# Kernel optimization log

Hardware: AMD Instinct MI355X
Metric: run time of the kernel (lower is better)

The kernel has to match this reference:

```python
import jax, jax.numpy as jnp
import numpy as np

B, T = 2, 2048
V, C, H = 32000, 1024, 16
HS = C // H  # 64
W_SCALE = 0.02


def setup_inputs() -> dict:
    key = jax.random.key(0)
    ks = jax.random.split(key, 8)
    x = jax.random.randint(ks[0], (B, T), 0, V)
    tok_emb = jax.random.normal(ks[1], (V, C), jnp.float32) * W_SCALE
    pos_emb = jax.random.normal(ks[2], (T, C), jnp.float32) * W_SCALE
    wq = jax.random.normal(ks[3], (H, C, HS), jnp.float32) * W_SCALE
    wk = jax.random.normal(ks[4], (H, C, HS), jnp.float32) * W_SCALE
    wv = jax.random.normal(ks[5], (H, C, HS), jnp.float32) * W_SCALE
    bq = jnp.zeros((H, HS), jnp.float32)
    bk = jnp.zeros((H, HS), jnp.float32)
    bv = jnp.zeros((H, HS), jnp.float32)
    w_head = jax.random.normal(ks[6], (C, V), jnp.float32) * W_SCALE
    b_head = jnp.zeros((V,), jnp.float32)
    return dict(x=x, tok_emb=tok_emb, pos_emb=pos_emb, wq=wq, bq=bq,
                wk=wk, bk=bk, wv=wv, bv=bv, w_head=w_head, b_head=b_head)


def reference(x, tok_emb, pos_emb, wq, bq, wk, bk, wv, bv, w_head, b_head):
    Bx, Tx = x.shape
    Cx = tok_emb.shape[1]
    h = tok_emb[x] + pos_emb[:Tx]  # [B,T,C]
    # all heads batched: per-head Linear layers stacked on leading H axis
    q = jnp.einsum('btc,hcd->bhtd', h, wq) + bq[None, :, None, :]
    k = jnp.einsum('btc,hcd->bhtd', h, wk) + bk[None, :, None, :]
    v = jnp.einsum('btc,hcd->bhtd', h, wv) + bv[None, :, None, :]
    # NOTE: original scales by n_embd**-0.5 (full C), not head_size**-0.5
    att = jnp.einsum('bhtd,bhsd->bhts', q, k) * (Cx ** -0.5)
    causal = jnp.tril(jnp.ones((Tx, Tx), dtype=bool))
    att = jnp.where(causal, att, jnp.finfo(att.dtype).min)
    att = jax.nn.softmax(att, axis=-1)
    y = jnp.einsum('bhts,bhsd->bhtd', att, v)  # [B,H,T,HS]
    y = jnp.transpose(y, (0, 2, 1, 3)).reshape(Bx, Tx, Cx)  # concat heads
    logits = jnp.einsum('btc,cv->btv', y, w_head) + b_head  # [B,T,V]
    return logits
```

## Files before the change

### kernel.cpp

```cpp
#include <hip/hip_runtime.h>

#define T_SEQ 2048
#define C_DIM 1024
#define H_N   16
#define HS_D  64
#define V_DIM 32000

typedef float f32x4 __attribute__((ext_vector_type(4)));
typedef __bf16 bf16x8 __attribute__((ext_vector_type(8)));
typedef unsigned short us4 __attribute__((ext_vector_type(4)));
typedef unsigned short us8 __attribute__((ext_vector_type(8)));

__device__ inline unsigned short f2bf(float f) {
  unsigned int u = __float_as_uint(f);
  u = (u + 0x7FFFu + ((u >> 16) & 1u)) >> 16;
  return (unsigned short)u;
}

__global__ __launch_bounds__(256) void embed_kernel(
    const int* __restrict__ x, const float* __restrict__ tok,
    const float* __restrict__ pos, unsigned short* __restrict__ h) {
  int idx = blockIdx.x * 256 + threadIdx.x;
  int bt = idx >> 8;
  int c4 = (idx & 255) * 4;
  int t = bt & (T_SEQ - 1);
  int tokid = x[bt];
  f32x4 a = *(const f32x4*)(tok + (size_t)tokid * C_DIM + c4);
  f32x4 b = *(const f32x4*)(pos + (size_t)t * C_DIM + c4);
  f32x4 s = a + b;
  us4 o;
  o[0] = f2bf(s[0]); o[1] = f2bf(s[1]); o[2] = f2bf(s[2]); o[3] = f2bf(s[3]);
  *(us4*)(h + (size_t)bt * C_DIM + c4) = o;
}

__global__ __launch_bounds__(256) void repack_qkv(
    const float* __restrict__ wq, const float* __restrict__ wk, const float* __restrict__ wv,
    const float* __restrict__ bq, const float* __restrict__ bk, const float* __restrict__ bv,
    unsigned short* __restrict__ wt, float* __restrict__ biasp) {
  int which = blockIdx.y;
  const float* w = (which == 0) ? wq : (which == 1) ? wk : wv;
  int i = blockIdx.x * 256 + threadIdx.x;
  int d = i & 63;
  int c = (i >> 6) & (C_DIM - 1);
  int hh = i >> 16;
  int n = which * 1024 + hh * 64 + d;
  wt[(size_t)n * C_DIM + c] = f2bf(w[i]);
  if (c == 0) {
    const float* bb = (which == 0) ? bq : (which == 1) ? bk : bv;
    biasp[n] = bb[hh * 64 + d];
  }
}

__global__ __launch_bounds__(256) void repack_whead(
    const float* __restrict__ wh, unsigned short* __restrict__ wht) {
  __shared__ float tile[64][65];
  int v0 = blockIdx.x * 64;
  int c0 = blockIdx.y * 64;
  int tr = threadIdx.x >> 6;
  int tc = threadIdx.x & 63;
#pragma unroll
  for (int i = 0; i < 16; ++i) {
    int r = i * 4 + tr;
    tile[r][tc] = wh[(size_t)(c0 + r) * V_DIM + v0 + tc];
  }
  __syncthreads();
#pragma unroll
  for (int i = 0; i < 16; ++i) {
    int vr = i * 4 + tr;
    wht[(size_t)(v0 + vr) * C_DIM + c0 + tc] = f2bf(tile[tc][vr]);
  }
}

__global__ __launch_bounds__(256) void gemm_bf16_o16(
    const unsigned short* __restrict__ A, const unsigned short* __restrict__ Bt,
    const float* __restrict__ bias, unsigned short* __restrict__ Cout, int N, int Mtiles) {
  const int K = 1024;
  __shared__ unsigned short As[128 * 32];
  __shared__ unsigned short Bs[128 * 32];
  int tid = threadIdx.x;
  int lane = tid & 63, wvi = tid >> 6;
  int cpx = gridDim.x >> 3;
  int lin = blockIdx.x;
  int wg = (lin & 7) * cpx + (lin >> 3);
  int m0 = (wg % Mtiles) * 128;
  int n0 = (wg / Mtiles) * 128;
  int wmm = (wvi >> 1) * 64, wnn = (wvi & 1) * 64;
  int r16 = lane & 15, gg = lane >> 4;
  f32x4 acc[4][4] = {};

  for (int k0 = 0; k0 < K; k0 += 32) {
#pragma unroll
    for (int it = 0; it < 2; ++it) {
      int ch = it * 256 + wvi * 64 + lane;
      int row = ch >> 2, cc = (ch & 3) * 8;
      const unsigned short* ga = A + (size_t)(m0 + row) * K + k0 + cc;
      __builtin_amdgcn_global_load_lds(
          (const __attribute__((address_space(1))) void*)ga,
          (__attribute__((address_space(3))) void*)&As[ch * 8], 16, 0, 0);
      const unsigned short* gb = Bt + (size_t)(n0 + row) * K + k0 + cc;
      __builtin_amdgcn_global_load_lds(
          (const __attribute__((address_space(1))) void*)gb,
          (__attribute__((address_space(3))) void*)&Bs[ch * 8], 16, 0, 0);
    }
    __syncthreads();
    bf16x8 fa[4], fb[4];
#pragma unroll
    for (int m = 0; m < 4; ++m)
      fa[m] = *(const bf16x8*)&As[(wmm + m * 16 + r16) * 32 + gg * 8];
#pragma unroll
    for (int n = 0; n < 4; ++n)
      fb[n] = *(const bf16x8*)&Bs[(wnn + n * 16 + r16) * 32 + gg * 8];
#pragma unroll
    for (int m = 0; m < 4; ++m)
#pragma unroll
      for (int n = 0; n < 4; ++n)
        acc[m][n] = __builtin_amdgcn_mfma_f32_16x16x32_bf16(fa[m], fb[n], acc[m][n], 0, 0, 0);
    __syncthreads();
  }
#pragma unroll
  for (int m = 0; m < 4; ++m) {
    int row = m0 + wmm + m * 16 + gg * 4;
#pragma unroll
    for (int n = 0; n < 4; ++n) {
      int col = n0 + wnn + n * 16 + r16;
      float bval = bias[col];
#pragma unroll
      for (int j = 0; j < 4; ++j)
        Cout[(size_t)(row + j) * N + col] = f2bf(acc[m][n][j] + bval);
    }
  }
}

__global__ __launch_bounds__(256) void transpose_v(
    const unsigned short* __restrict__ qkv, unsigned short* __restrict__ vt) {
  __shared__ unsigned short tile[64][72];
  int bh = blockIdx.y;
  int b = bh >> 4, h = bh & 15;
  int tb = blockIdx.x;
  int r = threadIdx.x >> 2;
  int c0 = (threadIdx.x & 3) * 16;
  const unsigned short* src = qkv + ((size_t)(b * T_SEQ) + tb * 64 + r) * 3072 + 2048 + h * 64 + c0;
  *(us8*)&tile[r][c0] = *(const us8*)src;
  *(us8*)&tile[r][c0 + 8] = *(const us8*)(src + 8);
  __syncthreads();
  unsigned short* dst = vt + (size_t)bh * 64 * T_SEQ + (size_t)r * T_SEQ + tb * 64 + c0;
  us8 o1, o2;
#pragma unroll
  for (int i = 0; i < 8; ++i) { o1[i] = tile[c0 + i][r]; o2[i] = tile[c0 + 8 + i][r]; }
  *(us8*)dst = o1;
  *(us8*)(dst + 8) = o2;
}

#define GK 1024
#define GNT 16

__global__ __launch_bounds__(512, 1) void gemm256(
    const unsigned short* __restrict__ A, const unsigned short* __restrict__ Bt,
    const float* __restrict__ bias, float* __restrict__ Cout, int N, int Mtiles) {
  __shared__ unsigned short As[2][256 * 64];
  __shared__ unsigned short Bs[2][256 * 64];
  int tid = threadIdx.x;
  int lane = tid & 63;
  int wid = tid >> 6;
  int wm = wid >> 2, wn = wid & 3;
  int l16 = lane & 15, g = lane >> 4;
  int swz = l16 & 7;

  int cpx = gridDim.x >> 3;
  int lin = blockIdx.x;
  int wg = (lin & 7) * cpx + (lin >> 3);
  int m0 = (wg % Mtiles) * 256;
  int n0 = (wg / Mtiles) * 256;

  auto stageA2 = [&](int kt, int mh) {
    unsigned short* lds = As[kt & 1];
#pragma unroll
    for (int q = 0; q < 2; ++q) {
      int chunk = q * 512 + tid;
      int rr = chunk >> 3;
      int row = (rr & 63) + ((rr >> 6) << 7) + mh * 64;
      int cpos = chunk & 7;
      int c = cpos ^ (row & 7);
      const unsigned short* src = A + (size_t)(m0 + row) * GK + kt * 64 + c * 8;
      __builtin_amdgcn_global_load_lds(
          (const __attribute__((address_space(1))) void*)src,
          (__attribute__((address_space(3))) void*)(lds + row * 64 + cpos * 8), 16, 0, 0);
    }
  };
  auto stageB4 = [&](int kt) {
    unsigned short* lds = Bs[kt & 1];
#pragma unroll
    for (int q = 0; q < 4; ++q) {
      int chunk = q * 512 + tid;
      int row = chunk >> 3;
      int cpos = chunk & 7;
      int c = cpos ^ (row & 7);
      const unsigned short* src = Bt + (size_t)(n0 + row) * GK + kt * 64 + c * 8;
      __builtin_amdgcn_global_load_lds(
          (const __attribute__((address_space(1))) void*)src,
          (__attribute__((address_space(3))) void*)(lds + row * 64 + cpos * 8), 16, 0, 0);
    }
  };

  stageA2(0, 0); stageB4(0);
  stageA2(0, 1);
  stageA2(1, 0); stageB4(1);
  asm volatile("s_waitcnt vmcnt(8)" ::: "memory");
  asm volatile("s_barrier" ::: "memory");

  f32x4 acc[8][4] = {};

  for (int t = 0; t < GNT; ++t) {
    const char* Ab = (const char*)As[t & 1];
    const char* Bb = (const char*)Bs[t & 1];
    bf16x8 bA[4][2], bB[4][2];

#pragma unroll
    for (int mi = 0; mi < 4; ++mi) {
      int row = wm * 128 + mi * 16 + l16;
#pragma unroll
      for (int kk = 0; kk < 2; ++kk)
        bA[mi][kk] = *(const bf16x8*)(Ab + row * 128 + (((kk * 4 + g) ^ swz) * 16));
    }
#pragma unroll
    for (int ni = 0; ni < 4; ++ni) {
      int row = wn * 64 + ni * 16 + l16;
#pragma unroll
      for (int kk = 0; kk < 2; ++kk)
        bB[ni][kk] = *(const bf16x8*)(Bb + row * 128 + (((kk * 4 + g) ^ swz) * 16));
    }
    if (t + 1 < GNT) stageA2(t + 1, 1);
    asm volatile("s_barrier" ::: "memory");
    asm volatile("s_waitcnt lgkmcnt(0)" ::: "memory");
    __builtin_amdgcn_sched_barrier(0);
    __builtin_amdgcn_s_setprio(1);
#pragma unroll
    for (int mi = 0; mi < 4; ++mi)
#pragma unroll
      for (int ni = 0; ni < 4; ++ni)
#pragma unroll
        for (int kk = 0; kk < 2; ++kk)
          acc[mi][ni] = __builtin_amdgcn_mfma_f32_16x16x32_bf16(bB[ni][kk], bA[mi][kk], acc[mi][ni], 0, 0, 0);
    __builtin_amdgcn_s_setprio(0);
    if (t + 1 < GNT) asm volatile("s_waitcnt vmcnt(8)" ::: "memory");
    else             asm volatile("s_waitcnt vmcnt(0)" ::: "memory");
    asm volatile("s_barrier" ::: "memory");

#pragma unroll
    for (int mi = 0; mi < 4; ++mi) {
      int row = wm * 128 + 64 + mi * 16 + l16;
#pragma unroll
      for (int kk = 0; kk < 2; ++kk)
        bA[mi][kk] = *(const bf16x8*)(Ab + row * 128 + (((kk * 4 + g) ^ swz) * 16));
    }
    if (t + 2 < GNT) { stageA2(t + 2, 0); stageB4(t + 2); }
    asm volatile("s_barrier" ::: "memory");
    asm volatile("s_waitcnt lgkmcnt(0)" ::: "memory");
    __builtin_amdgcn_sched_barrier(0);
    __builtin_amdgcn_s_setprio(1);
#pragma unroll
    for (int mi = 0; mi < 4; ++mi)
#pragma unroll
      for (int ni = 0; ni < 4; ++ni)
#pragma unroll
        for (int kk = 0; kk < 2; ++kk)
          acc[4 + mi][ni] = __builtin_amdgcn_mfma_f32_16x16x32_bf16(bB[ni][kk], bA[mi][kk], acc[4 + mi][ni], 0, 0, 0);
    __builtin_amdgcn_s_setprio(0);
    if (t + 2 < GNT)       asm volatile("s_waitcnt vmcnt(8)" ::: "memory");
    else if (t + 2 == GNT) asm volatile("s_waitcnt vmcnt(2)" ::: "memory");
    asm volatile("s_barrier" ::: "memory");
  }

#pragma unroll
  for (int mf = 0; mf < 8; ++mf) {
    int row = m0 + wm * 128 + mf * 16 + l16;
    float* outp = Cout + (size_t)row * N + n0 + wn * 64;
#pragma unroll
    for (int ni = 0; ni < 4; ++ni) {
      f32x4 v = acc[mf][ni];
      f32x4 bv = *(const f32x4*)&bias[n0 + wn * 64 + ni * 16 + g * 4];
      v += bv;
      __builtin_nontemporal_store(v, (f32x4*)(outp + ni * 16 + g * 4));
    }
  }
}

__global__ __launch_bounds__(256) void attn_mfma(
    const unsigned short* __restrict__ qkv, const unsigned short* __restrict__ vt,
    unsigned short* __restrict__ y) {
  __shared__ unsigned short Kl[2][4096];
  __shared__ unsigned short Vl[2][4096];
  __shared__ char Pl[8192];

  int bh = blockIdx.y;
  int b = bh >> 4, h = bh & 15;
  int qb = (T_SEQ / 64 - 1) - blockIdx.x;
  int tid = threadIdx.x;
  int lane = tid & 63, w = tid >> 6;
  int l16 = lane & 15, g = lane >> 4;
  size_t bT = (size_t)b * T_SEQ;
  const float scale2 = 0.03125f * 1.44269504f;

  const unsigned short* qrow = qkv + (bT + qb * 64 + w * 16 + l16) * 3072 + h * 64;
  bf16x8 qf[2] = { *(const bf16x8*)(qrow + g * 8), *(const bf16x8*)(qrow + 32 + g * 8) };

  f32x4 yacc[4] = {};
  float mrun[4], lrun[4];
#pragma unroll
  for (int j = 0; j < 4; ++j) { mrun[j] = -3.0e38f; lrun[j] = 0.f; }

  auto stageK = [&](int kb, int buf) {
    const unsigned short* base = qkv + (bT + kb * 64) * 3072 + 1024 + h * 64;
#pragma unroll
    for (int q2 = 0; q2 < 2; ++q2) {
      int chunk = q2 * 256 + tid;
      int row = chunk >> 3, cpos = chunk & 7;
      int c = cpos ^ (row & 7);
      const unsigned short* src = base + (size_t)row * 3072 + c * 8;
      __builtin_amdgcn_global_load_lds(
          (const __attribute__((address_space(1))) void*)src,
          (__attribute__((address_space(3))) void*)&Kl[buf][chunk * 8], 16, 0, 0);
    }
  };
  auto stageV = [&](int kb, int buf) {
    const unsigned short* base = vt + (size_t)bh * 64 * T_SEQ + kb * 64;
#pragma unroll
    for (int q2 = 0; q2 < 2; ++q2) {
      int chunk = q2 * 256 + tid;
      int row = chunk >> 3, cpos = chunk & 7;
      int c = cpos ^ (row & 7);
      const unsigned short* src = base + (size_t)row * T_SEQ + c * 8;
      __builtin_amdgcn_global_load_lds(
          (const __attribute__((address_space(1))) void*)src,
          (__attribute__((address_space(3))) void*)&Vl[buf][chunk * 8], 16, 0, 0);
    }
  };

  stageK(0, 0); stageV(0, 0);

  for (int kb = 0; kb <= qb; ++kb) {
    int buf = kb & 1;
    if (kb < qb) { stageK(kb + 1, buf ^ 1); stageV(kb + 1, buf ^ 1); }
    if (kb < qb) asm volatile("s_waitcnt vmcnt(4)" ::: "memory");
    else         asm volatile("s_waitcnt vmcnt(0)" ::: "memory");
    asm volatile("s_barrier" ::: "memory");

    f32x4 s[4] = {};
#pragma unroll
    for (int kk = 0; kk < 2; ++kk)
#pragma unroll
      for (int n = 0; n < 4; ++n) {
        int krow = n * 16 + l16;
        bf16x8 fb = *(const bf16x8*)((const char*)Kl[buf] + krow * 128 + (((kk * 4 + g) ^ (krow & 7)) * 16));
        s[n] = __builtin_amdgcn_mfma_f32_16x16x32_bf16(qf[kk], fb, s[n], 0, 0, 0);
      }

    bool diag = (kb == qb);
    float pr[4][4];
    float corr[4];
#pragma unroll
    for (int j = 0; j < 4; ++j) {
      int rloc = w * 16 + g * 4 + j;
      float m = -3.0e38f;
#pragma unroll
      for (int n = 0; n < 4; ++n) {
        float v = s[n][j] * scale2;
        if (diag && (n * 16 + l16) > rloc) v = -3.0e38f;
        pr[n][j] = v;
        m = fmaxf(m, v);
      }
      m = fmaxf(m, __shfl_xor(m, 1));
      m = fmaxf(m, __shfl_xor(m, 2));
      m = fmaxf(m, __shfl_xor(m, 4));
      m = fmaxf(m, __shfl_xor(m, 8));
      float mn = fmaxf(mrun[j], m);
      corr[j] = exp2f(mrun[j] - mn);
      mrun[j] = mn;
      float ps = 0.f;
#pragma unroll
      for (int n = 0; n < 4; ++n) {
        float e = exp2f(pr[n][j] - mn);
        pr[n][j] = e;
        ps += e;
      }
      ps += __shfl_xor(ps, 1);
      ps += __shfl_xor(ps, 2);
      ps += __shfl_xor(ps, 4);
      ps += __shfl_xor(ps, 8);
      lrun[j] = lrun[j] * corr[j] + ps;
    }
#pragma unroll
    for (int n = 0; n < 4; ++n)
#pragma unroll
      for (int j = 0; j < 4; ++j)
        yacc[n][j] *= corr[j];

#pragma unroll
    for (int j = 0; j < 4; ++j) {
      int row = w * 16 + g * 4 + j;
#pragma unroll
      for (int n = 0; n < 4; ++n)
        *(unsigned short*)(Pl + ((row * 128 + (n * 16 + l16) * 2) ^ ((row & 7) << 4))) = f2bf(pr[n][j]);
    }

#pragma unroll
    for (int kk = 0; kk < 2; ++kk) {
      int prow = w * 16 + l16;
      bf16x8 fa = *(const bf16x8*)(Pl + ((prow * 128 + (kk * 32 + g * 8) * 2) ^ ((prow & 7) << 4)));
#pragma unroll
      for (int n = 0; n < 4; ++n) {
        int vrow = n * 16 + l16;
        bf16x8 fbv = *(const bf16x8*)((const char*)Vl[buf] + vrow * 128 + (((kk * 4 + g) ^ (vrow & 7)) * 16));
        yacc[n] = __builtin_amdgcn_mfma_f32_16x16x32_bf16(fa, fbv, yacc[n], 0, 0, 0);
      }
    }
    asm volatile("s_barrier" ::: "memory");
  }

#pragma unroll
  for (int j = 0; j < 4; ++j) {
    float inv = 1.0f / lrun[j];
    int row = qb * 64 + w * 16 + g * 4 + j;
    unsigned short* yo = y + (bT + row) * C_DIM + h * 64;
#pragma unroll
    for (int n = 0; n < 4; ++n)
      yo[n * 16 + l16] = f2bf(yacc[n][j] * inv);
  }
}

extern "C" void kernel_launch(void* const* d_in, const int* in_sizes, int n_in,
                              void* d_out, int out_size, void* d_ws, size_t ws_size,
                              hipStream_t stream) {
  const int*   x    = (const int*)d_in[0];
  const float* tok  = (const float*)d_in[1];
  const float* pos  = (const float*)d_in[2];
  const float* wq   = (const float*)d_in[3];
  const float* bq   = (const float*)d_in[4];
  const float* wk   = (const float*)d_in[5];
  const float* bk   = (const float*)d_in[6];
  const float* wv   = (const float*)d_in[7];
  const float* bv   = (const float*)d_in[8];
  const float* wh   = (const float*)d_in[9];
  const float* bhd  = (const float*)d_in[10];
  float* out = (float*)d_out;

  char* ws = (char*)d_ws;
  size_t off = 0;
  auto alloc = [&](size_t bytes) {
    void* p = ws + off;
    off += (bytes + 255) & ~(size_t)255;
    return p;
  };
  unsigned short* h_bf    = (unsigned short*)alloc((size_t)4096 * 1024 * 2);
  unsigned short* wqkv_t  = (unsigned short*)alloc((size_t)3072 * 1024 * 2);
  float*          qbias   = (float*)alloc((size_t)3072 * 4);
  unsigned short* wh_t    = (unsigned short*)alloc((size_t)V_DIM * 1024 * 2);
  unsigned short* qkv_bf  = (unsigned short*)alloc((size_t)4096 * 3072 * 2);
  unsigned short* vtb     = (unsigned short*)alloc((size_t)32 * 64 * T_SEQ * 2);
  unsigned short* ybf     = (unsigned short*)alloc((size_t)4096 * 1024 * 2);

  embed_kernel<<<4096, 256, 0, stream>>>(x, tok, pos, h_bf);
  repack_qkv<<<dim3(4096, 3), 256, 0, stream>>>(wq, wk, wv, bq, bk, bv, wqkv_t, qbias);
  repack_whead<<<dim3(V_DIM / 64, 16), 256, 0, stream>>>(wh, wh_t);
  gemm_bf16_o16<<<768, 256, 0, stream>>>(h_bf, wqkv_t, qbias, qkv_bf, 3072, 32);
  transpose_v<<<dim3(T_SEQ / 64, 2 * H_N), 256, 0, stream>>>(qkv_bf, vtb);
  attn_mfma<<<dim3(T_SEQ / 64, 2 * H_N), 256, 0, stream>>>(qkv_bf, vtb, ybf);
  gemm256<<<2000, 512, 0, stream>>>(ybf, wh_t, bhd, out, V_DIM, 16);
}
```

Measured before the change: 566.4 us.

## Restructure gemm256 main loop into eight-phase quarter-tile schedule with finer prefetch

Replaces the two-phase per-K-step loop of the 256x256 GEMM with an unrolled schedule of eight phases per two K-steps. Each phase reads a half of A or B fragments, issues a half-tile global-to-LDS prefetch and runs 16 MFMAs, reusing register fragments across quadrants in a snake order. The goal is to interleave LDS reads, async global loads and MFMA work more finely so memory latency is hidden behind compute. The loop count is hardcoded to 8 iterations (16 K-steps), which assumes GK=1024. The output store also changes from nontemporal to a regular store, and the extra barriers add synchronisation overhead.

```diff
diff --git a/kernel.cpp b/kernel.cpp
--- a/kernel.cpp
+++ b/kernel.cpp
@@ -172,102 +172,129 @@
   int m0 = (wg % Mtiles) * 256;
   int n0 = (wg / Mtiles) * 256;
 
-  auto stageA2 = [&](int kt, int mh) {
-    unsigned short* lds = As[kt & 1];
+  auto stageH = [&](const unsigned short* __restrict__ G, int base,
+                    unsigned short* lds, int kt, int h) {
 #pragma unroll
     for (int q = 0; q < 2; ++q) {
       int chunk = q * 512 + tid;
-      int rr = chunk >> 3;
-      int row = (rr & 63) + ((rr >> 6) << 7) + mh * 64;
+      int rowl = chunk >> 3;
+      int row = h * 128 + rowl;
       int cpos = chunk & 7;
       int c = cpos ^ (row & 7);
-      const unsigned short* src = A + (size_t)(m0 + row) * GK + kt * 64 + c * 8;
+      const unsigned short* src = G + (size_t)(base + row) * GK + kt * 64 + c * 8;
       __builtin_amdgcn_global_load_lds(
           (const __attribute__((address_space(1))) void*)src,
           (__attribute__((address_space(3))) void*)(lds + row * 64 + cpos * 8), 16, 0, 0);
     }
   };
-  auto stageB4 = [&](int kt) {
-    unsigned short* lds = Bs[kt & 1];
-#pragma unroll
-    for (int q = 0; q < 4; ++q) {
-      int chunk = q * 512 + tid;
-      int row = chunk >> 3;
-      int cpos = chunk & 7;
-      int c = cpos ^ (row & 7);
-      const unsigned short* src = Bt + (size_t)(n0 + row) * GK + kt * 64 + c * 8;
-      __builtin_amdgcn_global_load_lds(
-          (const __attribute__((address_space(1))) void*)src,
-          (__attribute__((address_space(3))) void*)(lds + row * 64 + cpos * 8), 16, 0, 0);
-    }
-  };
-
-  stageA2(0, 0); stageB4(0);
-  stageA2(0, 1);
-  stageA2(1, 0); stageB4(1);
-  asm volatile("s_waitcnt vmcnt(8)" ::: "memory");
+
+  stageH(Bt, n0, Bs[0], 0, 0); stageH(Bt, n0, Bs[0], 0, 1);
+  stageH(A,  m0, As[0], 0, 0); stageH(A,  m0, As[0], 0, 1);
+  stageH(Bt, n0, Bs[1], 1, 0); stageH(Bt, n0, Bs[1], 1, 1);
+  asm volatile("s_waitcnt vmcnt(4)" ::: "memory");
   asm volatile("s_barrier" ::: "memory");
 
   f32x4 acc[8][4] = {};
-
-  for (int t = 0; t < GNT; ++t) {
-    const char* Ab = (const char*)As[t & 1];
-    const char* Bb = (const char*)Bs[t & 1];
-    bf16x8 bA[4][2], bB[4][2];
-
+  bf16x8 bA[4][2], bB[4][2];
+
+  auto readA = [&](const char* Ab, int mh) {
 #pragma unroll
     for (int mi = 0; mi < 4; ++mi) {
-      int row = wm * 128 + mi * 16 + l16;
+      int row = wm * 128 + mh * 64 + mi * 16 + l16;
 #pragma unroll
       for (int kk = 0; kk < 2; ++kk)
         bA[mi][kk] = *(const bf16x8*)(Ab + row * 128 + (((kk * 4 + g) ^ swz) * 16));
     }
-#pragma unroll
-    for (int ni = 0; ni < 4; ++ni) {
-      int row = wn * 64 + ni * 16 + l16;
+  };
+  auto readB2 = [&](const char* Bb, int nh) {
+#pragma unroll
+    for (int ni = 0; ni < 2; ++ni) {
+      int row = wn * 64 + nh * 32 + ni * 16 + l16;
 #pragma unroll
       for (int kk = 0; kk < 2; ++kk)
-        bB[ni][kk] = *(const bf16x8*)(Bb + row * 128 + (((kk * 4 + g) ^ swz) * 16));
-    }
-    if (t + 1 < GNT) stageA2(t + 1, 1);
-    asm volatile("s_barrier" ::: "memory");
-    asm volatile("s_waitcnt lgkmcnt(0)" ::: "memory");
-    __builtin_amdgcn_sched_barrier(0);
-    __builtin_amdgcn_s_setprio(1);
+        bB[nh * 2 + ni][kk] = *(const bf16x8*)(Bb + row * 128 + (((kk * 4 + g) ^ swz) * 16));
+    }
+  };
+  auto mfma16 = [&](int a, int b) {
 #pragma unroll
     for (int mi = 0; mi < 4; ++mi)
 #pragma unroll
-      for (int ni = 0; ni < 4; ++ni)
+      for (int ni = 0; ni < 2; ++ni)
 #pragma unroll
         for (int kk = 0; kk < 2; ++kk)
-          acc[mi][ni] = __builtin_amdgcn_mfma_f32_16x16x32_bf16(bB[ni][kk], bA[mi][kk], acc[mi][ni], 0, 0, 0);
-    __builtin_amdgcn_s_setprio(0);
-    if (t + 1 < GNT) asm volatile("s_waitcnt vmcnt(8)" ::: "memory");
-    else             asm volatile("s_waitcnt vmcnt(0)" ::: "memory");
-    asm volatile("s_barrier" ::: "memory");
-
-#pragma unroll
-    for (int mi = 0; mi < 4; ++mi) {
-      int row = wm * 128 + 64 + mi * 16 + l16;
-#pragma unroll
-      for (int kk = 0; kk < 2; ++kk)
-        bA[mi][kk] = *(const bf16x8*)(Ab + row * 128 + (((kk * 4 + g) ^ swz) * 16));
-    }
-    if (t + 2 < GNT) { stageA2(t + 2, 0); stageB4(t + 2); }
-    asm volatile("s_barrier" ::: "memory");
-    asm volatile("s_waitcnt lgkmcnt(0)" ::: "memory");
-    __builtin_amdgcn_sched_barrier(0);
-    __builtin_amdgcn_s_setprio(1);
-#pragma unroll
-    for (int mi = 0; mi < 4; ++mi)
-#pragma unroll
-      for (int ni = 0; ni < 4; ++ni)
-#pragma unroll
-        for (int kk = 0; kk < 2; ++kk)
-          acc[4 + mi][ni] = __builtin_amdgcn_mfma_f32_16x16x32_bf16(bB[ni][kk], bA[mi][kk], acc[4 + mi][ni], 0, 0, 0);
-    __builtin_amdgcn_s_setprio(0);
-    if (t + 2 < GNT)       asm volatile("s_waitcnt vmcnt(8)" ::: "memory");
-    else if (t + 2 == GNT) asm volatile("s_waitcnt vmcnt(2)" ::: "memory");
+          acc[4 * a + mi][2 * b + ni] = __builtin_amdgcn_mfma_f32_16x16x32_bf16(
+              bB[2 * b + ni][kk], bA[mi][kk], acc[4 * a + mi][2 * b + ni], 0, 0, 0);
+  };
+
+  for (int it = 0; it < 8; ++it) {
+    int u = 2 * it;
+    bool pf = (it < 7);
+    const char* A0 = (const char*)As[0];
+    const char* B0 = (const char*)Bs[0];
+    const char* A1 = (const char*)As[1];
+    const char* B1 = (const char*)Bs[1];
+
+    readA(A0, 0); readB2(B0, 0);
+    stageH(A, m0, As[1], u + 1, 0);
+    asm volatile("s_waitcnt lgkmcnt(8)" ::: "memory");
+    asm volatile("s_barrier" ::: "memory");
+    asm volatile("s_waitcnt lgkmcnt(0)" ::: "memory");
+    __builtin_amdgcn_sched_barrier(0);
+    __builtin_amdgcn_s_setprio(1); mfma16(0, 0); __builtin_amdgcn_s_setprio(0);
+    asm volatile("s_barrier" ::: "memory");
+
+    readB2(B0, 1);
+    stageH(A, m0, As[1], u + 1, 1);
+    asm volatile("s_barrier" ::: "memory");
+    asm volatile("s_waitcnt lgkmcnt(0)" ::: "memory");
+    __builtin_amdgcn_sched_barrier(0);
+    __builtin_amdgcn_s_setprio(1); mfma16(0, 1); __builtin_amdgcn_s_setprio(0);
+    asm volatile("s_barrier" ::: "memory");
+
+    readA(A0, 1);
+    if (pf) stageH(Bt, n0, Bs[0], u + 2, 0);
+    asm volatile("s_barrier" ::: "memory");
+    asm volatile("s_waitcnt lgkmcnt(0)" ::: "memory");
+    __builtin_amdgcn_sched_barrier(0);
+    __builtin_amdgcn_s_setprio(1); mfma16(1, 1); __builtin_amdgcn_s_setprio(0);
+    asm volatile("s_barrier" ::: "memory");
+
+    if (pf) stageH(Bt, n0, Bs[0], u + 2, 1);
+    asm volatile("s_barrier" ::: "memory");
+    __builtin_amdgcn_s_setprio(1); mfma16(1, 0); __builtin_amdgcn_s_setprio(0);
+    if (pf) asm volatile("s_waitcnt vmcnt(4)" ::: "memory");
+    else    asm volatile("s_waitcnt vmcnt(0)" ::: "memory");
+    asm volatile("s_barrier" ::: "memory");
+
+    readA(A1, 0); readB2(B1, 0);
+    if (pf) stageH(A, m0, As[0], u + 2, 0);
+    asm volatile("s_waitcnt lgkmcnt(8)" ::: "memory");
+    asm volatile("s_barrier" ::: "memory");
+    asm volatile("s_waitcnt lgkmcnt(0)" ::: "memory");
+    __builtin_amdgcn_sched_barrier(0);
+    __builtin_amdgcn_s_setprio(1); mfma16(0, 0); __builtin_amdgcn_s_setprio(0);
+    asm volatile("s_barrier" ::: "memory");
+
+    readB2(B1, 1);
+    if (pf) stageH(A, m0, As[0], u + 2, 1);
+    asm volatile("s_barrier" ::: "memory");
+    asm volatile("s_waitcnt lgkmcnt(0)" ::: "memory");
+    __builtin_amdgcn_sched_barrier(0);
+    __builtin_amdgcn_s_setprio(1); mfma16(0, 1); __builtin_amdgcn_s_setprio(0);
+    asm volatile("s_barrier" ::: "memory");
+
+    readA(A1, 1);
+    if (pf) stageH(Bt, n0, Bs[1], u + 3, 0);
+    asm volatile("s_barrier" ::: "memory");
+    asm volatile("s_waitcnt lgkmcnt(0)" ::: "memory");
+    __builtin_amdgcn_sched_barrier(0);
+    __builtin_amdgcn_s_setprio(1); mfma16(1, 1); __builtin_amdgcn_s_setprio(0);
+    asm volatile("s_barrier" ::: "memory");
+
+    if (pf) stageH(Bt, n0, Bs[1], u + 3, 1);
+    asm volatile("s_barrier" ::: "memory");
+    __builtin_amdgcn_s_setprio(1); mfma16(1, 0); __builtin_amdgcn_s_setprio(0);
+    if (pf) asm volatile("s_waitcnt vmcnt(4)" ::: "memory");
     asm volatile("s_barrier" ::: "memory");
   }
 
@@ -280,7 +307,7 @@
       f32x4 v = acc[mf][ni];
       f32x4 bv = *(const f32x4*)&bias[n0 + wn * 64 + ni * 16 + g * 4];
       v += bv;
-      __builtin_nontemporal_store(v, (f32x4*)(outp + ni * 16 + g * 4));
+      *(f32x4*)(outp + ni * 16 + g * 4) = v;
     }
   }
 }
```

After: 612.0 us. 8.1% more time.
